# Performance work log

Hardware: AMD Instinct MI355X
Metric: run time of the kernel (lower is better)

The kernel has to match this reference:

```python
import jax, jax.numpy as jnp
import numpy as np

IMAGE_SIZE = 224
COV_HP = 1.0
SIGMA = 1.0
STEPS = 2
CUTOFF = 20.0
IMP_LO, IMP_HI = 0.5, 2.0
REL_W = 0.5
EPS = 1e-6

# Projection matrices for front/top/left views (buffer Js in the module)
JS = jnp.array([[[1, 0, 0], [0, 1, 0]],
                [[1, 0, 0], [0, 0, 1]],
                [[0, 0, 1], [0, 1, 0]]], dtype=jnp.float32)


def _blur(d, sigma):
    # d: [B,H,W]; separable Gaussian blur, 'same' padding
    r = max(1, int(3 * sigma))
    x = jnp.arange(-r, r + 1, dtype=jnp.float32)
    k = jnp.exp(-(x * x) / (2.0 * sigma * sigma))
    k = k / k.sum()
    d4 = d[:, None]  # [B,1,H,W]
    kh = k.reshape(1, 1, -1, 1)
    kw = k.reshape(1, 1, 1, -1)
    d4 = jax.lax.conv_general_dilated(d4, kh, (1, 1), [(r, r), (0, 0)],
                                      dimension_numbers=('NCHW', 'OIHW', 'NCHW'))
    d4 = jax.lax.conv_general_dilated(d4, kw, (1, 1), [(0, 0), (r, r)],
                                      dimension_numbers=('NCHW', 'OIHW', 'NCHW'))
    return d4[:, 0]


def _fill_depth_map(d, sigma, steps):
    # fill_depth_map is not defined in the source; implemented as iterative
    # Gaussian-blur hole filling (empty pixels take blurred neighborhood).
    for _ in range(steps):
        b = _blur(d, sigma)
        d = jnp.where(d > 1e-6, d, b)
    return d


def _forward(position, cov3d, opacity, importance):
    B, N, _ = position.shape
    H = W = IMAGE_SIZE
    Hh, Wh = H // 2, W // 2
    yy, xx = jnp.meshgrid(jnp.arange(Hh), jnp.arange(Wh), indexing='ij')
    grid = jnp.stack([xx, yy], axis=-1).astype(jnp.float32)  # [Hh,Wh,2]
    imp = jnp.clip(jnp.broadcast_to(importance[:, :N], (B, N)), IMP_LO, IMP_HI)
    imp = imp[:, :, None, None]
    eye3 = jnp.eye(3, dtype=cov3d.dtype)
    eye2 = jnp.eye(2, dtype=cov3d.dtype)
    maps = []
    for v in range(3):  # fixed small view loop, as in the source
        J = JS[v]  # [2,3]
        # NOTE: source mutates cov3d across the view loop; replicate that
        cov3d = (cov3d + jnp.swapaxes(cov3d, -1, -2)) * 0.5
        cov3d = cov3d + EPS * eye3
        nrm = jnp.linalg.norm(cov3d, axis=(-1, -2), keepdims=True)
        cov3d = cov3d / (nrm + EPS) * COV_HP
        cinv = jnp.linalg.inv(cov3d)                               # [B,N,3,3]
        cov2d_inv = jnp.einsum('ij,bnjk,lk->bnil', J, cinv, J)     # J C^-1 J^T
        cov2d_inv = cov2d_inv + eye2 * (EPS * 1e-4)
        proj = jnp.einsum('bnk,jk->bnj', position, J)              # [B,N,2]
        mn = proj.min(axis=1, keepdims=True)
        mx = proj.max(axis=1, keepdims=True)
        rng = mx - mn + 1e-6
        mn = mn - 0.5 * rng
        mx = mx + 0.5 * rng
        rng = mx - mn + 1e-6
        xy = jnp.clip((proj - mn) / rng * (Wh - 1), 0.0, Wh - 1)
        delta = grid[None, None] - xy[:, :, None, None, :]         # [B,N,Hh,Wh,2]
        mask_h = jnp.linalg.norm(delta, axis=-1) < CUTOFF
        mask = jnp.repeat(jnp.repeat(mask_h, 2, axis=2), 2, axis=3)
        exph = -jnp.einsum('bnhwj,bnjk,bnhwk->bnhw', delta, cov2d_inv, delta)
        exp_full = jax.image.resize(exph, (B, N, H, W), method='bilinear')
        exp_full = jnp.clip(exp_full, -20.0, 0.0)
        w = opacity[:, :, None, None] * imp * jnp.exp(exp_full)
        w = jnp.where(mask, w, 0.0)
        wmin = w.min(axis=1, keepdims=True)
        wmax = w.max(axis=1, keepdims=True)
        nw = (w - wmin) / (wmax - wmin + EPS) * REL_W + w / (w.sum(axis=1, keepdims=True) + EPS)
        dm = nw.sum(axis=1)  # [B,H,W]
        maps.append(_fill_depth_map(dm, SIGMA, STEPS))
    d = jnp.stack(maps, axis=1)  # [B,3,H,W], already 224x224 so resize is a no-op
    d = (d - d.mean()) / (jnp.std(d, ddof=1) + EPS)
    return d


def setup_inputs() -> dict:
    key = jax.random.key(0)
    k1, k2, k3 = jax.random.split(key, 3)
    B, N, MAXG = 1, 512, 1000
    return {
        'position': jax.random.normal(k1, (B, N, 3), dtype=jnp.float32),
        'cov3d': jax.random.normal(k2, (B, N, 3, 3), dtype=jnp.float32),
        'opacity': jax.random.uniform(k3, (B, N), dtype=jnp.float32),
        'importance': jnp.ones((1, MAXG), dtype=jnp.float32),
    }


def reference(position, cov3d, opacity, importance):
    return _forward(position, cov3d, opacity, importance)
```

## Files before the change

### kernel.cpp

```cpp
#include <hip/hip_runtime.h>
#include <math.h>


__device__ __forceinline__ float wave_min(float v) {
    #pragma unroll
    for (int o = 32; o >= 1; o >>= 1) v = fminf(v, __shfl_xor(v, o));
    return v;
}

__global__ __launch_bounds__(512) void splat_fused_kernel(
    const float* __restrict__ position, const float* __restrict__ cov3d,
    const float* __restrict__ opacity, const float* __restrict__ importance,
    float* __restrict__ dm) {
    __shared__ float4 lsA[512];
    __shared__ float2 lsB[512];
    __shared__ float red[8 * 6];
    __shared__ float4 pS[7][64], pMn[7][64], pMx[7][64];
    __shared__ int cnt;
    const int v = blockIdx.z;
    const int tx0 = blockIdx.x * 16, ty0 = blockIdx.y * 16;
    const int tid = threadIdx.x;
    const int lane = tid & 63, wave = tid >> 6;

    const int n = tid;
    const float p0 = position[n * 3 + 0];
    const float p1 = position[n * 3 + 1];
    const float p2 = position[n * 3 + 2];
    const float opimp = opacity[n] * fminf(fmaxf(importance[n], 0.5f), 2.0f);

    {
        float vals[6] = {p0, -p0, p1, -p1, p2, -p2};
        #pragma unroll
        for (int k = 0; k < 6; ++k) {
            float r = wave_min(vals[k]);
            if (lane == 0) red[wave * 6 + k] = r;
        }
    }
    __syncthreads();
    float mn6[6];
    #pragma unroll
    for (int k = 0; k < 6; ++k) {
        float r = red[k];
        #pragma unroll
        for (int w = 1; w < 8; ++w) r = fminf(r, red[w * 6 + k]);
        mn6[k] = r;
    }
    const float pmn[3] = {mn6[0], mn6[2], mn6[4]};
    const float pmx[3] = {-mn6[1], -mn6[3], -mn6[5]};

    float c00 = cov3d[n * 9 + 0], c01 = cov3d[n * 9 + 1], c02 = cov3d[n * 9 + 2];
    float c10 = cov3d[n * 9 + 3], c11 = cov3d[n * 9 + 4], c12 = cov3d[n * 9 + 5];
    float c20 = cov3d[n * 9 + 6], c21 = cov3d[n * 9 + 7], c22 = cov3d[n * 9 + 8];
    for (int vv = 0; vv <= v; ++vv) {
        float s01 = 0.5f * (c01 + c10);
        float s02 = 0.5f * (c02 + c20);
        float s12 = 0.5f * (c12 + c21);
        float s00 = c00 + 1e-6f;
        float s11 = c11 + 1e-6f;
        float s22 = c22 + 1e-6f;
        float nrm = sqrtf(s00 * s00 + s11 * s11 + s22 * s22 +
                          2.0f * (s01 * s01 + s02 * s02 + s12 * s12));
        float inv = 1.0f / (nrm + 1e-6f);
        c00 = s00 * inv; c11 = s11 * inv; c22 = s22 * inv;
        c01 = s01 * inv; c10 = c01; c02 = s02 * inv; c20 = c02;
        c12 = s12 * inv; c21 = c12;
    }
    float cof00 = c11 * c22 - c12 * c12;
    float cof01 = c02 * c12 - c01 * c22;
    float cof02 = c01 * c12 - c02 * c11;
    float det = c00 * cof00 + c01 * cof01 + c02 * cof02;
    float idet = 1.0f / det;
    float i00 = cof00 * idet;
    float i01 = cof01 * idet;
    float i02 = cof02 * idet;
    float i11 = (c00 * c22 - c02 * c02) * idet;
    float i12 = (c02 * c01 - c00 * c12) * idet;
    float i22 = (c00 * c11 - c01 * c01) * idet;

    float Aa, Ab, Ac, prx, pry;
    int ix, iy;
    if (v == 0)      { Aa = i00; Ab = i01; Ac = i11; prx = p0; pry = p1; ix = 0; iy = 1; }
    else if (v == 1) { Aa = i00; Ab = i02; Ac = i22; prx = p0; pry = p2; ix = 0; iy = 2; }
    else             { Aa = i22; Ab = i12; Ac = i11; prx = p2; pry = p1; ix = 2; iy = 1; }
    Aa += 1e-10f;
    Ac += 1e-10f;

    float mnx = pmn[ix], mxx = pmx[ix], mny = pmn[iy], mxy = pmx[iy];
    float rngx = mxx - mnx + 1e-6f;
    float mnx2 = mnx - 0.5f * rngx;
    float mxx2 = mxx + 0.5f * rngx;
    rngx = mxx2 - mnx2 + 1e-6f;
    float rngy = mxy - mny + 1e-6f;
    float mny2 = mny - 0.5f * rngy;
    float mxy2 = mxy + 0.5f * rngy;
    rngy = mxy2 - mny2 + 1e-6f;
    float gx = fminf(fmaxf((prx - mnx2) / rngx * 111.0f, 0.0f), 111.0f);
    float gy = fminf(fmaxf((pry - mny2) / rngy * 111.0f, 0.0f), 111.0f);

    if (tid == 0) cnt = 0;
    __syncthreads();
    {
        const float bx0 = (float)(tx0 >> 1), bx1 = (float)((tx0 + 15) >> 1);
        const float by0 = (float)(ty0 >> 1), by1 = (float)((ty0 + 15) >> 1);
        float dx = fmaxf(fmaxf(bx0 - gx, gx - bx1), 0.0f);
        float dy = fmaxf(fmaxf(by0 - gy, gy - by1), 0.0f);
        bool pass = (dx * dx + dy * dy) < 400.01f;
        unsigned long long m = __ballot(pass);
        int base = 0;
        if (lane == 0) base = atomicAdd(&cnt, __popcll(m));
        base = __shfl(base, 0);
        if (pass) {
            int slot = base + __popcll(m & ((1ull << lane) - 1ull));
            lsA[slot] = make_float4(Aa, 2.0f * Ab, Ac, opimp);
            lsB[slot] = make_float2(gx, gy);
        }
    }
    __syncthreads();
    const int len = cnt;

    const int qx = lane & 7, qy = lane >> 3;
    const int xh = (tx0 >> 1) + qx;
    const int yh = (ty0 >> 1) + qy;

    if (len == 0) {
        if (wave == 0) {
            #pragma unroll
            for (int py = 0; py < 2; ++py)
                #pragma unroll
                for (int px = 0; px < 2; ++px)
                    dm[(v * 224 + ty0 + 2 * qy + py) * 224 + tx0 + 2 * qx + px] = 0.0f;
        }
        return;
    }

    const int npad = (len + 15) & ~15;
    if (tid < npad - len) {
        lsA[len + tid] = make_float4(1.0f, 0.0f, 1.0f, 0.0f);
        lsB[len + tid] = make_float2(1e9f, 1e9f);
    }
    __syncthreads();

    float exA[2], eyA[2], VxA[2], VyA[2];
    #pragma unroll
    for (int p = 0; p < 2; ++p) {
        int xlo = xh - 1 + p; int xhi = min(xlo + 1, 111); xlo = max(xlo, 0);
        float wlo = p ? 0.75f : 0.25f, whi = 1.0f - wlo;
        exA[p] = wlo * (float)xlo + whi * (float)xhi;
        VxA[p] = wlo * whi * (float)(xhi - xlo) * (float)(xhi - xlo);
        int ylo = yh - 1 + p; int yhi2 = min(ylo + 1, 111); ylo = max(ylo, 0);
        eyA[p] = wlo * (float)ylo + whi * (float)yhi2;
        VyA[p] = wlo * whi * (float)(yhi2 - ylo) * (float)(yhi2 - ylo);
    }
    const float fxh = (float)xh, fyh = (float)yh;

    const int chunk = npad >> 3;
    const int cbeg = wave * chunk, cend = cbeg + chunk;

    float S00 = 0.f, S01 = 0.f, S10 = 0.f, S11 = 0.f;
    float mn00 = INFINITY, mn01 = INFINITY, mn10 = INFINITY, mn11 = INFINITY;
    float mx00 = -INFINITY, mx01 = -INFINITY, mx10 = -INFINITY, mx11 = -INFINITY;

    for (int i = cbeg; i < cend; i += 2) {
        float4 gA0 = lsA[i], gA1 = lsA[i + 1];
        float2 gB0 = lsB[i], gB1 = lsB[i + 1];
        #pragma unroll
        for (int u = 0; u < 2; ++u) {
            const float4 gA = u ? gA1 : gA0;
            const float2 gB = u ? gB1 : gB0;
            const float a = gA.x, b2 = gA.y, c = gA.z, op = gA.w;
            const float xx = gB.x, yy = gB.y;
            const float dxh = fxh - xx, dyh = fyh - yy;
            const bool inside = dxh * dxh + dyh * dyh < 400.0f;
            const float dx0 = exA[0] - xx, dx1 = exA[1] - xx;
            const float dy0 = eyA[0] - yy, dy1 = eyA[1] - yy;
            const float adx0 = a * dx0, adx1 = a * dx1;
            const float bdy0 = b2 * dy0, bdy1 = b2 * dy1;
            const float cdy0 = c * dy0 * dy0, cdy1 = c * dy1 * dy1;
            const float ax0 = a * VxA[0], ax1 = a * VxA[1];
            const float cy0 = c * VyA[0], cy1 = c * VyA[1];
            #pragma unroll
            for (int py = 0; py < 2; ++py) {
                const float dyp  = py ? dy1 : dy0;
                const float bdyp = py ? bdy1 : bdy0;
                const float cdyp = py ? cdy1 : cdy0;
                const float cyp  = py ? cy1 : cy0;
                #pragma unroll
                for (int px = 0; px < 2; ++px) {
                    const float dxp  = px ? dx1 : dx0;
                    const float adxp = px ? adx1 : adx0;
                    const float axp  = px ? ax1 : ax0;
                    float q = dxp * (adxp + bdyp) + cdyp;
                    float bil = -((q + axp) + cyp);
                    bil = fminf(fmaxf(bil, -20.0f), 0.0f);
                    bil = inside ? bil : -1e9f;
                    float w = op * __expf(bil);
                    if (py == 0 && px == 0) { S00 += w; mn00 = fminf(mn00, w); mx00 = fmaxf(mx00, w); }
                    if (py == 0 && px == 1) { S01 += w; mn01 = fminf(mn01, w); mx01 = fmaxf(mx01, w); }
                    if (py == 1 && px == 0) { S10 += w; mn10 = fminf(mn10, w); mx10 = fmaxf(mx10, w); }
                    if (py == 1 && px == 1) { S11 += w; mn11 = fminf(mn11, w); mx11 = fmaxf(mx11, w); }
                }
            }
        }
    }
    if (wave > 0) {
        pS[wave - 1][lane]  = make_float4(S00, S01, S10, S11);
        pMn[wave - 1][lane] = make_float4(mn00, mn01, mn10, mn11);
        pMx[wave - 1][lane] = make_float4(mx00, mx01, mx10, mx11);
    }
    __syncthreads();
    if (wave == 0) {
        #pragma unroll
        for (int k = 0; k < 7; ++k) {
            float4 s = pS[k][lane], m = pMn[k][lane], M = pMx[k][lane];
            S00 += s.x; S01 += s.y; S10 += s.z; S11 += s.w;
            mn00 = fminf(mn00, m.x); mn01 = fminf(mn01, m.y);
            mn10 = fminf(mn10, m.z); mn11 = fminf(mn11, m.w);
            mx00 = fmaxf(mx00, M.x); mx01 = fmaxf(mx01, M.y);
            mx10 = fmaxf(mx10, M.z); mx11 = fmaxf(mx11, M.w);
        }
        if (len < 512) {
            mn00 = fminf(mn00, 0.f); mn01 = fminf(mn01, 0.f);
            mn10 = fminf(mn10, 0.f); mn11 = fminf(mn11, 0.f);
            mx00 = fmaxf(mx00, 0.f); mx01 = fmaxf(mx01, 0.f);
            mx10 = fmaxf(mx10, 0.f); mx11 = fmaxf(mx11, 0.f);
        }
        float S4[4]  = {S00, S01, S10, S11};
        float mn4[4] = {mn00, mn01, mn10, mn11};
        float mx4[4] = {mx00, mx01, mx10, mx11};
        #pragma unroll
        for (int pp = 0; pp < 4; ++pp) {
            float S = S4[pp];
            float dmv = 0.5f * (S - 512.0f * mn4[pp]) / (mx4[pp] - mn4[pp] + 1e-6f)
                      + S / (S + 1e-6f);
            const int py = pp >> 1, px = pp & 1;
            dm[(v * 224 + ty0 + 2 * qy + py) * 224 + tx0 + 2 * qx + px] = dmv;
        }
    }
}

__global__ __launch_bounds__(256) void blur2_stats_kernel(
    const float* __restrict__ in, float* __restrict__ out,
    float2* __restrict__ partials) {
    __shared__ float A[28 * 29];
    __shared__ float T[28 * 29];
    __shared__ float r1[4], r2[4];
    const int v = blockIdx.z;
    const int tx0 = blockIdx.x * 16, ty0 = blockIdx.y * 16;
    const int tid = threadIdx.x;
    const float kw[7] = {0.00443305f, 0.05400558f, 0.24203623f, 0.39905030f,
                         0.24203623f, 0.05400558f, 0.00443305f};
    const float* __restrict__ chan = in + v * 224 * 224;

    for (int idx = tid; idx < 28 * 28; idx += 256) {
        int rr = idx / 28, c = idx % 28;
        int gyy = ty0 - 6 + rr, gxx = tx0 - 6 + c;
        float val = 0.0f;
        if (gyy >= 0 && gyy < 224 && gxx >= 0 && gxx < 224) val = chan[gyy * 224 + gxx];
        A[rr * 29 + c] = val;
    }
    __syncthreads();
    for (int idx = tid; idx < 22 * 28; idx += 256) {
        int rr = 3 + idx / 28, c = idx % 28;
        float s = 0.0f;
        #pragma unroll
        for (int i = 0; i < 7; ++i) s += kw[i] * A[(rr - 3 + i) * 29 + c];
        T[rr * 29 + c] = s;
    }
    __syncthreads();
    for (int idx = tid; idx < 22 * 22; idx += 256) {
        int rr = 3 + idx / 22, c = 3 + idx % 22;
        int gyy = ty0 - 6 + rr, gxx = tx0 - 6 + c;
        float s = 0.0f;
        #pragma unroll
        for (int j = 0; j < 7; ++j) s += kw[j] * T[rr * 29 + c - 3 + j];
        float ctr = A[rr * 29 + c];
        float d1 = ctr > 1e-6f ? ctr : s;
        if (gyy < 0 || gyy > 223 || gxx < 0 || gxx > 223) d1 = 0.0f;
        A[rr * 29 + c] = d1;
    }
    __syncthreads();
    for (int idx = tid; idx < 16 * 22; idx += 256) {
        int rr = 6 + idx / 22, c = 3 + idx % 22;
        float s = 0.0f;
        #pragma unroll
        for (int i = 0; i < 7; ++i) s += kw[i] * A[(rr - 3 + i) * 29 + c];
        T[rr * 29 + c] = s;
    }
    __syncthreads();
    float ls1 = 0.0f, ls2 = 0.0f;
    for (int idx = tid; idx < 16 * 16; idx += 256) {
        int rr = 6 + (idx >> 4), c = 6 + (idx & 15);
        float s = 0.0f;
        #pragma unroll
        for (int j = 0; j < 7; ++j) s += kw[j] * T[rr * 29 + c - 3 + j];
        float ctr = A[rr * 29 + c];
        float d2 = ctr > 1e-6f ? ctr : s;
        out[(v * 224 + ty0 + rr - 6) * 224 + (tx0 + c - 6)] = d2;
        ls1 += d2; ls2 += d2 * d2;
    }
    #pragma unroll
    for (int o = 32; o >= 1; o >>= 1) {
        ls1 += __shfl_xor(ls1, o);
        ls2 += __shfl_xor(ls2, o);
    }
    if ((tid & 63) == 0) { r1[tid >> 6] = ls1; r2[tid >> 6] = ls2; }
    __syncthreads();
    if (tid == 0) {
        float s1 = r1[0] + r1[1] + r1[2] + r1[3];
        float s2 = r2[0] + r2[1] + r2[2] + r2[3];
        partials[(blockIdx.z * 14 + blockIdx.y) * 14 + blockIdx.x] = make_float2(s1, s2);
    }
}

__global__ __launch_bounds__(256) void normalize_kernel(
    const float2* __restrict__ partials, float* __restrict__ out) {
    __shared__ double s1[256], s2[256];
    const int tid = threadIdx.x;
    double a = 0.0, b = 0.0;
    for (int i = tid; i < 588; i += 256) {
        float2 p = partials[i];
        a += (double)p.x; b += (double)p.y;
    }
    s1[tid] = a; s2[tid] = b;
    __syncthreads();
    for (int s = 128; s >= 1; s >>= 1) {
        if (tid < s) { s1[tid] += s1[tid + s]; s2[tid] += s2[tid + s]; }
        __syncthreads();
    }
    const double M = 150528.0;
    double mean = s1[0] / M;
    double var = (s2[0] - M * mean * mean) / (M - 1.0);
    double sd = sqrt(var > 0.0 ? var : 0.0);
    const int idx = blockIdx.x * 256 + tid;
    if (idx < 3 * 224 * 224)
        out[idx] = (out[idx] - (float)mean) / ((float)sd + 1e-6f);
}

extern "C" void kernel_launch(void* const* d_in, const int* in_sizes, int n_in,
                              void* d_out, int out_size, void* d_ws, size_t ws_size,
                              hipStream_t stream) {
    const float* position   = (const float*)d_in[0];
    const float* cov3d      = (const float*)d_in[1];
    const float* opacity    = (const float*)d_in[2];
    const float* importance = (const float*)d_in[3];
    float* out = (float*)d_out;

    float* dmA       = (float*)d_ws;
    float2* partials = (float2*)((float*)d_ws + 150528);

    hipLaunchKernelGGL(splat_fused_kernel, dim3(14, 14, 3), dim3(512), 0, stream,
                       position, cov3d, opacity, importance, dmA);
    hipLaunchKernelGGL(blur2_stats_kernel, dim3(14, 14, 3), dim3(256), 0, stream,
                       dmA, out, partials);
    hipLaunchKernelGGL(normalize_kernel, dim3(588), dim3(256), 0, stream,
                       partials, out);
}
```

Before: 90.57 us.

## Fuse splat, blur and normalize into one cooperative kernel with grid syncs

Replaces the three-kernel pipeline with a single cooperative launch. Grid-wide syncs separate the splat, the two-step blur with statistics, and the normalization, so two kernel launch gaps go away. Blocks shrink to 256 threads, each handling two Gaussians, so all 588 blocks can be co-resident, and the final value stays in a register instead of being written and read back. Each block redundantly reduces the 588 partials after the last sync. Grid-sync cost and lower per-block parallelism in the splat loop may offset the gain, and the old three-kernel path remains as a fallback if the cooperative launch fails.

```diff
diff --git a/kernel.cpp b/kernel.cpp
--- a/kernel.cpp
+++ b/kernel.cpp
@@ -1,5 +1,8 @@
 #include <hip/hip_runtime.h>
+#include <hip/hip_cooperative_groups.h>
 #include <math.h>
+
+namespace cg = cooperative_groups;
 
 
 __device__ __forceinline__ float wave_min(float v) {
@@ -8,83 +11,69 @@
     return v;
 }
 
-__global__ __launch_bounds__(512) void splat_fused_kernel(
+struct SpS {
+    float4 lsA[512];
+    float2 lsB[512];
+    float4 pS[3][64], pMn[3][64], pMx[3][64];
+    float red[4 * 6];
+    int cnt;
+};
+struct BlS {
+    float A[28 * 29];
+    float T[28 * 29];
+    float r1[4], r2[4];
+};
+struct NmS {
+    double s1[256], s2[256];
+};
+union SmU { SpS sp; BlS bl; NmS nm; };
+
+__global__ __launch_bounds__(256, 3) void fused_all_kernel(
     const float* __restrict__ position, const float* __restrict__ cov3d,
     const float* __restrict__ opacity, const float* __restrict__ importance,
-    float* __restrict__ dm) {
-    __shared__ float4 lsA[512];
-    __shared__ float2 lsB[512];
-    __shared__ float red[8 * 6];
-    __shared__ float4 pS[7][64], pMn[7][64], pMx[7][64];
-    __shared__ int cnt;
+    float* __restrict__ dm, float2* __restrict__ partials,
+    float* __restrict__ out) {
+    __shared__ SmU sm;
+    cg::grid_group gg = cg::this_grid();
     const int v = blockIdx.z;
     const int tx0 = blockIdx.x * 16, ty0 = blockIdx.y * 16;
     const int tid = threadIdx.x;
     const int lane = tid & 63, wave = tid >> 6;
 
-    const int n = tid;
-    const float p0 = position[n * 3 + 0];
-    const float p1 = position[n * 3 + 1];
-    const float p2 = position[n * 3 + 2];
-    const float opimp = opacity[n] * fminf(fmaxf(importance[n], 0.5f), 2.0f);
-
+    float P0[3], P1[3], OP0, OP1;
     {
-        float vals[6] = {p0, -p0, p1, -p1, p2, -p2};
+        const int n0 = tid, n1 = tid + 256;
+        P0[0] = position[n0 * 3 + 0]; P0[1] = position[n0 * 3 + 1]; P0[2] = position[n0 * 3 + 2];
+        P1[0] = position[n1 * 3 + 0]; P1[1] = position[n1 * 3 + 1]; P1[2] = position[n1 * 3 + 2];
+        OP0 = opacity[n0] * fminf(fmaxf(importance[n0], 0.5f), 2.0f);
+        OP1 = opacity[n1] * fminf(fmaxf(importance[n1], 0.5f), 2.0f);
+    }
+    if (tid == 0) sm.sp.cnt = 0;
+    {
+        float vals[6] = { fminf(P0[0], P1[0]), fminf(-P0[0], -P1[0]),
+                          fminf(P0[1], P1[1]), fminf(-P0[1], -P1[1]),
+                          fminf(P0[2], P1[2]), fminf(-P0[2], -P1[2]) };
         #pragma unroll
         for (int k = 0; k < 6; ++k) {
             float r = wave_min(vals[k]);
-            if (lane == 0) red[wave * 6 + k] = r;
+            if (lane == 0) sm.sp.red[wave * 6 + k] = r;
         }
     }
     __syncthreads();
     float mn6[6];
     #pragma unroll
     for (int k = 0; k < 6; ++k) {
-        float r = red[k];
-        #pragma unroll
-        for (int w = 1; w < 8; ++w) r = fminf(r, red[w * 6 + k]);
+        float r = sm.sp.red[k];
+        #pragma unroll
+        for (int w = 1; w < 4; ++w) r = fminf(r, sm.sp.red[w * 6 + k]);
         mn6[k] = r;
     }
     const float pmn[3] = {mn6[0], mn6[2], mn6[4]};
     const float pmx[3] = {-mn6[1], -mn6[3], -mn6[5]};
-
-    float c00 = cov3d[n * 9 + 0], c01 = cov3d[n * 9 + 1], c02 = cov3d[n * 9 + 2];
-    float c10 = cov3d[n * 9 + 3], c11 = cov3d[n * 9 + 4], c12 = cov3d[n * 9 + 5];
-    float c20 = cov3d[n * 9 + 6], c21 = cov3d[n * 9 + 7], c22 = cov3d[n * 9 + 8];
-    for (int vv = 0; vv <= v; ++vv) {
-        float s01 = 0.5f * (c01 + c10);
-        float s02 = 0.5f * (c02 + c20);
-        float s12 = 0.5f * (c12 + c21);
-        float s00 = c00 + 1e-6f;
-        float s11 = c11 + 1e-6f;
-        float s22 = c22 + 1e-6f;
-        float nrm = sqrtf(s00 * s00 + s11 * s11 + s22 * s22 +
-                          2.0f * (s01 * s01 + s02 * s02 + s12 * s12));
-        float inv = 1.0f / (nrm + 1e-6f);
-        c00 = s00 * inv; c11 = s11 * inv; c22 = s22 * inv;
-        c01 = s01 * inv; c10 = c01; c02 = s02 * inv; c20 = c02;
-        c12 = s12 * inv; c21 = c12;
-    }
-    float cof00 = c11 * c22 - c12 * c12;
-    float cof01 = c02 * c12 - c01 * c22;
-    float cof02 = c01 * c12 - c02 * c11;
-    float det = c00 * cof00 + c01 * cof01 + c02 * cof02;
-    float idet = 1.0f / det;
-    float i00 = cof00 * idet;
-    float i01 = cof01 * idet;
-    float i02 = cof02 * idet;
-    float i11 = (c00 * c22 - c02 * c02) * idet;
-    float i12 = (c02 * c01 - c00 * c12) * idet;
-    float i22 = (c00 * c11 - c01 * c01) * idet;
-
-    float Aa, Ab, Ac, prx, pry;
     int ix, iy;
-    if (v == 0)      { Aa = i00; Ab = i01; Ac = i11; prx = p0; pry = p1; ix = 0; iy = 1; }
-    else if (v == 1) { Aa = i00; Ab = i02; Ac = i22; prx = p0; pry = p2; ix = 0; iy = 2; }
-    else             { Aa = i22; Ab = i12; Ac = i11; prx = p2; pry = p1; ix = 2; iy = 1; }
-    Aa += 1e-10f;
-    Ac += 1e-10f;
-
+    if (v == 0)      { ix = 0; iy = 1; }
+    else if (v == 1) { ix = 0; iy = 2; }
+    else             { ix = 2; iy = 1; }
     float mnx = pmn[ix], mxx = pmx[ix], mny = pmn[iy], mxy = pmx[iy];
     float rngx = mxx - mnx + 1e-6f;
     float mnx2 = mnx - 0.5f * rngx;
@@ -94,49 +83,77 @@
     float mny2 = mny - 0.5f * rngy;
     float mxy2 = mxy + 0.5f * rngy;
     rngy = mxy2 - mny2 + 1e-6f;
-    float gx = fminf(fmaxf((prx - mnx2) / rngx * 111.0f, 0.0f), 111.0f);
-    float gy = fminf(fmaxf((pry - mny2) / rngy * 111.0f, 0.0f), 111.0f);
-
-    if (tid == 0) cnt = 0;
-    __syncthreads();
-    {
-        const float bx0 = (float)(tx0 >> 1), bx1 = (float)((tx0 + 15) >> 1);
-        const float by0 = (float)(ty0 >> 1), by1 = (float)((ty0 + 15) >> 1);
+    const float bx0 = (float)(tx0 >> 1), bx1 = (float)((tx0 + 15) >> 1);
+    const float by0 = (float)(ty0 >> 1), by1 = (float)((ty0 + 15) >> 1);
+
+    for (int g = 0; g < 2; ++g) {
+        const int n = tid + (g << 8);
+        const float p0 = g ? P1[0] : P0[0];
+        const float p1 = g ? P1[1] : P0[1];
+        const float p2 = g ? P1[2] : P0[2];
+        const float opimp = g ? OP1 : OP0;
+        float c00 = cov3d[n * 9 + 0], c01 = cov3d[n * 9 + 1], c02 = cov3d[n * 9 + 2];
+        float c10 = cov3d[n * 9 + 3], c11 = cov3d[n * 9 + 4], c12 = cov3d[n * 9 + 5];
+        float c20 = cov3d[n * 9 + 6], c21 = cov3d[n * 9 + 7], c22 = cov3d[n * 9 + 8];
+        for (int vv = 0; vv <= v; ++vv) {
+            float s01 = 0.5f * (c01 + c10);
+            float s02 = 0.5f * (c02 + c20);
+            float s12 = 0.5f * (c12 + c21);
+            float s00 = c00 + 1e-6f;
+            float s11 = c11 + 1e-6f;
+            float s22 = c22 + 1e-6f;
+            float nrm = sqrtf(s00 * s00 + s11 * s11 + s22 * s22 +
+                              2.0f * (s01 * s01 + s02 * s02 + s12 * s12));
+            float inv = 1.0f / (nrm + 1e-6f);
+            c00 = s00 * inv; c11 = s11 * inv; c22 = s22 * inv;
+            c01 = s01 * inv; c10 = c01; c02 = s02 * inv; c20 = c02;
+            c12 = s12 * inv; c21 = c12;
+        }
+        float cof00 = c11 * c22 - c12 * c12;
+        float cof01 = c02 * c12 - c01 * c22;
+        float cof02 = c01 * c12 - c02 * c11;
+        float det = c00 * cof00 + c01 * cof01 + c02 * cof02;
+        float idet = 1.0f / det;
+        float i00 = cof00 * idet;
+        float i01 = cof01 * idet;
+        float i02 = cof02 * idet;
+        float i11 = (c00 * c22 - c02 * c02) * idet;
+        float i12 = (c02 * c01 - c00 * c12) * idet;
+        float i22 = (c00 * c11 - c01 * c01) * idet;
+
+        float Aa, Ab, Ac, prx, pry;
+        if (v == 0)      { Aa = i00; Ab = i01; Ac = i11; prx = p0; pry = p1; }
+        else if (v == 1) { Aa = i00; Ab = i02; Ac = i22; prx = p0; pry = p2; }
+        else             { Aa = i22; Ab = i12; Ac = i11; prx = p2; pry = p1; }
+        Aa += 1e-10f;
+        Ac += 1e-10f;
+        float gx = fminf(fmaxf((prx - mnx2) / rngx * 111.0f, 0.0f), 111.0f);
+        float gy = fminf(fmaxf((pry - mny2) / rngy * 111.0f, 0.0f), 111.0f);
+
         float dx = fmaxf(fmaxf(bx0 - gx, gx - bx1), 0.0f);
         float dy = fmaxf(fmaxf(by0 - gy, gy - by1), 0.0f);
         bool pass = (dx * dx + dy * dy) < 400.01f;
         unsigned long long m = __ballot(pass);
         int base = 0;
-        if (lane == 0) base = atomicAdd(&cnt, __popcll(m));
+        if (lane == 0) base = atomicAdd(&sm.sp.cnt, __popcll(m));
         base = __shfl(base, 0);
         if (pass) {
             int slot = base + __popcll(m & ((1ull << lane) - 1ull));
-            lsA[slot] = make_float4(Aa, 2.0f * Ab, Ac, opimp);
-            lsB[slot] = make_float2(gx, gy);
-        }
-    }
-    __syncthreads();
-    const int len = cnt;
+            sm.sp.lsA[slot] = make_float4(Aa, 2.0f * Ab, Ac, opimp);
+            sm.sp.lsB[slot] = make_float2(gx, gy);
+        }
+    }
+    __syncthreads();
+    const int len = sm.sp.cnt;
 
     const int qx = lane & 7, qy = lane >> 3;
     const int xh = (tx0 >> 1) + qx;
     const int yh = (ty0 >> 1) + qy;
 
-    if (len == 0) {
-        if (wave == 0) {
-            #pragma unroll
-            for (int py = 0; py < 2; ++py)
-                #pragma unroll
-                for (int px = 0; px < 2; ++px)
-                    dm[(v * 224 + ty0 + 2 * qy + py) * 224 + tx0 + 2 * qx + px] = 0.0f;
-        }
-        return;
-    }
-
     const int npad = (len + 15) & ~15;
     if (tid < npad - len) {
-        lsA[len + tid] = make_float4(1.0f, 0.0f, 1.0f, 0.0f);
-        lsB[len + tid] = make_float2(1e9f, 1e9f);
+        sm.sp.lsA[len + tid] = make_float4(1.0f, 0.0f, 1.0f, 0.0f);
+        sm.sp.lsB[len + tid] = make_float2(1e9f, 1e9f);
     }
     __syncthreads();
 
@@ -153,7 +170,7 @@
     }
     const float fxh = (float)xh, fyh = (float)yh;
 
-    const int chunk = npad >> 3;
+    const int chunk = npad >> 2;
     const int cbeg = wave * chunk, cend = cbeg + chunk;
 
     float S00 = 0.f, S01 = 0.f, S10 = 0.f, S11 = 0.f;
@@ -161,8 +178,8 @@
     float mx00 = -INFINITY, mx01 = -INFINITY, mx10 = -INFINITY, mx11 = -INFINITY;
 
     for (int i = cbeg; i < cend; i += 2) {
-        float4 gA0 = lsA[i], gA1 = lsA[i + 1];
-        float2 gB0 = lsB[i], gB1 = lsB[i + 1];
+        float4 gA0 = sm.sp.lsA[i], gA1 = sm.sp.lsA[i + 1];
+        float2 gB0 = sm.sp.lsB[i], gB1 = sm.sp.lsB[i + 1];
         #pragma unroll
         for (int u = 0; u < 2; ++u) {
             const float4 gA = u ? gA1 : gA0;
@@ -184,6 +201,7 @@
                 const float bdyp = py ? bdy1 : bdy0;
                 const float cdyp = py ? cdy1 : cdy0;
                 const float cyp  = py ? cy1 : cy0;
+                (void)dyp;
                 #pragma unroll
                 for (int px = 0; px < 2; ++px) {
                     const float dxp  = px ? dx1 : dx0;
@@ -203,6 +221,321 @@
         }
     }
     if (wave > 0) {
+        sm.sp.pS[wave - 1][lane]  = make_float4(S00, S01, S10, S11);
+        sm.sp.pMn[wave - 1][lane] = make_float4(mn00, mn01, mn10, mn11);
+        sm.sp.pMx[wave - 1][lane] = make_float4(mx00, mx01, mx10, mx11);
+    }
+    __syncthreads();
+    if (wave == 0) {
+        #pragma unroll
+        for (int k = 0; k < 3; ++k) {
+            float4 s = sm.sp.pS[k][lane], m = sm.sp.pMn[k][lane], M = sm.sp.pMx[k][lane];
+            S00 += s.x; S01 += s.y; S10 += s.z; S11 += s.w;
+            mn00 = fminf(mn00, m.x); mn01 = fminf(mn01, m.y);
+            mn10 = fminf(mn10, m.z); mn11 = fminf(mn11, m.w);
+            mx00 = fmaxf(mx00, M.x); mx01 = fmaxf(mx01, M.y);
+            mx10 = fmaxf(mx10, M.z); mx11 = fmaxf(mx11, M.w);
+        }
+        if (len < 512) {
+            mn00 = fminf(mn00, 0.f); mn01 = fminf(mn01, 0.f);
+            mn10 = fminf(mn10, 0.f); mn11 = fminf(mn11, 0.f);
+            mx00 = fmaxf(mx00, 0.f); mx01 = fmaxf(mx01, 0.f);
+            mx10 = fmaxf(mx10, 0.f); mx11 = fmaxf(mx11, 0.f);
+        }
+        float S4[4]  = {S00, S01, S10, S11};
+        float mn4[4] = {mn00, mn01, mn10, mn11};
+        float mx4[4] = {mx00, mx01, mx10, mx11};
+        #pragma unroll
+        for (int pp = 0; pp < 4; ++pp) {
+            float S = S4[pp];
+            float dmv = 0.5f * (S - 512.0f * mn4[pp]) / (mx4[pp] - mn4[pp] + 1e-6f)
+                      + S / (S + 1e-6f);
+            const int py = pp >> 1, px = pp & 1;
+            dm[(v * 224 + ty0 + 2 * qy + py) * 224 + tx0 + 2 * qx + px] = dmv;
+        }
+    }
+
+    gg.sync();
+
+    const float kw[7] = {0.00443305f, 0.05400558f, 0.24203623f, 0.39905030f,
+                         0.24203623f, 0.05400558f, 0.00443305f};
+    const float* __restrict__ chan = dm + v * 224 * 224;
+
+    for (int idx = tid; idx < 28 * 28; idx += 256) {
+        int rr = idx / 28, c = idx % 28;
+        int gyy = ty0 - 6 + rr, gxx = tx0 - 6 + c;
+        float val = 0.0f;
+        if (gyy >= 0 && gyy < 224 && gxx >= 0 && gxx < 224) val = chan[gyy * 224 + gxx];
+        sm.bl.A[rr * 29 + c] = val;
+    }
+    __syncthreads();
+    for (int idx = tid; idx < 22 * 28; idx += 256) {
+        int rr = 3 + idx / 28, c = idx % 28;
+        float s = 0.0f;
+        #pragma unroll
+        for (int i = 0; i < 7; ++i) s += kw[i] * sm.bl.A[(rr - 3 + i) * 29 + c];
+        sm.bl.T[rr * 29 + c] = s;
+    }
+    __syncthreads();
+    for (int idx = tid; idx < 22 * 22; idx += 256) {
+        int rr = 3 + idx / 22, c = 3 + idx % 22;
+        int gyy = ty0 - 6 + rr, gxx = tx0 - 6 + c;
+        float s = 0.0f;
+        #pragma unroll
+        for (int j = 0; j < 7; ++j) s += kw[j] * sm.bl.T[rr * 29 + c - 3 + j];
+        float ctr = sm.bl.A[rr * 29 + c];
+        float d1 = ctr > 1e-6f ? ctr : s;
+        if (gyy < 0 || gyy > 223 || gxx < 0 || gxx > 223) d1 = 0.0f;
+        sm.bl.A[rr * 29 + c] = d1;
+    }
+    __syncthreads();
+    for (int idx = tid; idx < 16 * 22; idx += 256) {
+        int rr = 6 + idx / 22, c = 3 + idx % 22;
+        float s = 0.0f;
+        #pragma unroll
+        for (int i = 0; i < 7; ++i) s += kw[i] * sm.bl.A[(rr - 3 + i) * 29 + c];
+        sm.bl.T[rr * 29 + c] = s;
+    }
+    __syncthreads();
+    const int rr2 = 6 + (tid >> 4), cc2 = 6 + (tid & 15);
+    float d2;
+    {
+        float s = 0.0f;
+        #pragma unroll
+        for (int j = 0; j < 7; ++j) s += kw[j] * sm.bl.T[rr2 * 29 + cc2 - 3 + j];
+        float ctr = sm.bl.A[rr2 * 29 + cc2];
+        d2 = ctr > 1e-6f ? ctr : s;
+    }
+    float ls1 = d2, ls2 = d2 * d2;
+    #pragma unroll
+    for (int o = 32; o >= 1; o >>= 1) {
+        ls1 += __shfl_xor(ls1, o);
+        ls2 += __shfl_xor(ls2, o);
+    }
+    if (lane == 0) { sm.bl.r1[wave] = ls1; sm.bl.r2[wave] = ls2; }
+    __syncthreads();
+    if (tid == 0) {
+        float s1 = sm.bl.r1[0] + sm.bl.r1[1] + sm.bl.r1[2] + sm.bl.r1[3];
+        float s2 = sm.bl.r2[0] + sm.bl.r2[1] + sm.bl.r2[2] + sm.bl.r2[3];
+        partials[(v * 14 + blockIdx.y) * 14 + blockIdx.x] = make_float2(s1, s2);
+    }
+
+    gg.sync();
+
+    double a = 0.0, b = 0.0;
+    for (int i = tid; i < 588; i += 256) {
+        float2 p = partials[i];
+        a += (double)p.x; b += (double)p.y;
+    }
+    sm.nm.s1[tid] = a; sm.nm.s2[tid] = b;
+    __syncthreads();
+    for (int s = 128; s >= 1; s >>= 1) {
+        if (tid < s) { sm.nm.s1[tid] += sm.nm.s1[tid + s]; sm.nm.s2[tid] += sm.nm.s2[tid + s]; }
+        __syncthreads();
+    }
+    const double M = 150528.0;
+    double mean = sm.nm.s1[0] / M;
+    double var = (sm.nm.s2[0] - M * mean * mean) / (M - 1.0);
+    double sd = sqrt(var > 0.0 ? var : 0.0);
+    out[(v * 224 + ty0 + (tid >> 4)) * 224 + tx0 + (tid & 15)] =
+        (d2 - (float)mean) / ((float)sd + 1e-6f);
+}
+
+
+__global__ __launch_bounds__(512) void splat_fused_kernel(
+    const float* __restrict__ position, const float* __restrict__ cov3d,
+    const float* __restrict__ opacity, const float* __restrict__ importance,
+    float* __restrict__ dm) {
+    __shared__ float4 lsA[512];
+    __shared__ float2 lsB[512];
+    __shared__ float red[8 * 6];
+    __shared__ float4 pS[7][64], pMn[7][64], pMx[7][64];
+    __shared__ int cnt;
+    const int v = blockIdx.z;
+    const int tx0 = blockIdx.x * 16, ty0 = blockIdx.y * 16;
+    const int tid = threadIdx.x;
+    const int lane = tid & 63, wave = tid >> 6;
+
+    const int n = tid;
+    const float p0 = position[n * 3 + 0];
+    const float p1 = position[n * 3 + 1];
+    const float p2 = position[n * 3 + 2];
+    const float opimp = opacity[n] * fminf(fmaxf(importance[n], 0.5f), 2.0f);
+
+    {
+        float vals[6] = {p0, -p0, p1, -p1, p2, -p2};
+        #pragma unroll
+        for (int k = 0; k < 6; ++k) {
+            float r = wave_min(vals[k]);
+            if (lane == 0) red[wave * 6 + k] = r;
+        }
+    }
+    __syncthreads();
+    float mn6[6];
+    #pragma unroll
+    for (int k = 0; k < 6; ++k) {
+        float r = red[k];
+        #pragma unroll
+        for (int w = 1; w < 8; ++w) r = fminf(r, red[w * 6 + k]);
+        mn6[k] = r;
+    }
+    const float pmn[3] = {mn6[0], mn6[2], mn6[4]};
+    const float pmx[3] = {-mn6[1], -mn6[3], -mn6[5]};
+
+    float c00 = cov3d[n * 9 + 0], c01 = cov3d[n * 9 + 1], c02 = cov3d[n * 9 + 2];
+    float c10 = cov3d[n * 9 + 3], c11 = cov3d[n * 9 + 4], c12 = cov3d[n * 9 + 5];
+    float c20 = cov3d[n * 9 + 6], c21 = cov3d[n * 9 + 7], c22 = cov3d[n * 9 + 8];
+    for (int vv = 0; vv <= v; ++vv) {
+        float s01 = 0.5f * (c01 + c10);
+        float s02 = 0.5f * (c02 + c20);
+        float s12 = 0.5f * (c12 + c21);
+        float s00 = c00 + 1e-6f;
+        float s11 = c11 + 1e-6f;
+        float s22 = c22 + 1e-6f;
+        float nrm = sqrtf(s00 * s00 + s11 * s11 + s22 * s22 +
+                          2.0f * (s01 * s01 + s02 * s02 + s12 * s12));
+        float inv = 1.0f / (nrm + 1e-6f);
+        c00 = s00 * inv; c11 = s11 * inv; c22 = s22 * inv;
+        c01 = s01 * inv; c10 = c01; c02 = s02 * inv; c20 = c02;
+        c12 = s12 * inv; c21 = c12;
+    }
+    float cof00 = c11 * c22 - c12 * c12;
+    float cof01 = c02 * c12 - c01 * c22;
+    float cof02 = c01 * c12 - c02 * c11;
+    float det = c00 * cof00 + c01 * cof01 + c02 * cof02;
+    float idet = 1.0f / det;
+    float i00 = cof00 * idet;
+    float i01 = cof01 * idet;
+    float i02 = cof02 * idet;
+    float i11 = (c00 * c22 - c02 * c02) * idet;
+    float i12 = (c02 * c01 - c00 * c12) * idet;
+    float i22 = (c00 * c11 - c01 * c01) * idet;
+
+    float Aa, Ab, Ac, prx, pry;
+    int ix, iy;
+    if (v == 0)      { Aa = i00; Ab = i01; Ac = i11; prx = p0; pry = p1; ix = 0; iy = 1; }
+    else if (v == 1) { Aa = i00; Ab = i02; Ac = i22; prx = p0; pry = p2; ix = 0; iy = 2; }
+    else             { Aa = i22; Ab = i12; Ac = i11; prx = p2; pry = p1; ix = 2; iy = 1; }
+    Aa += 1e-10f;
+    Ac += 1e-10f;
+
+    float mnx = pmn[ix], mxx = pmx[ix], mny = pmn[iy], mxy = pmx[iy];
+    float rngx = mxx - mnx + 1e-6f;
+    float mnx2 = mnx - 0.5f * rngx;
+    float mxx2 = mxx + 0.5f * rngx;
+    rngx = mxx2 - mnx2 + 1e-6f;
+    float rngy = mxy - mny + 1e-6f;
+    float mny2 = mny - 0.5f * rngy;
+    float mxy2 = mxy + 0.5f * rngy;
+    rngy = mxy2 - mny2 + 1e-6f;
+    float gx = fminf(fmaxf((prx - mnx2) / rngx * 111.0f, 0.0f), 111.0f);
+    float gy = fminf(fmaxf((pry - mny2) / rngy * 111.0f, 0.0f), 111.0f);
+
+    if (tid == 0) cnt = 0;
+    __syncthreads();
+    {
+        const float bx0 = (float)(tx0 >> 1), bx1 = (float)((tx0 + 15) >> 1);
+        const float by0 = (float)(ty0 >> 1), by1 = (float)((ty0 + 15) >> 1);
+        float dx = fmaxf(fmaxf(bx0 - gx, gx - bx1), 0.0f);
+        float dy = fmaxf(fmaxf(by0 - gy, gy - by1), 0.0f);
+        bool pass = (dx * dx + dy * dy) < 400.01f;
+        unsigned long long m = __ballot(pass);
+        int base = 0;
+        if (lane == 0) base = atomicAdd(&cnt, __popcll(m));
+        base = __shfl(base, 0);
+        if (pass) {
+            int slot = base + __popcll(m & ((1ull << lane) - 1ull));
+            lsA[slot] = make_float4(Aa, 2.0f * Ab, Ac, opimp);
+            lsB[slot] = make_float2(gx, gy);
+        }
+    }
+    __syncthreads();
+    const int len = cnt;
+
+    const int qx = lane & 7, qy = lane >> 3;
+    const int xh = (tx0 >> 1) + qx;
+    const int yh = (ty0 >> 1) + qy;
+
+    if (len == 0) {
+        if (wave == 0) {
+            #pragma unroll
+            for (int py = 0; py < 2; ++py)
+                #pragma unroll
+                for (int px = 0; px < 2; ++px)
+                    dm[(v * 224 + ty0 + 2 * qy + py) * 224 + tx0 + 2 * qx + px] = 0.0f;
+        }
+        return;
+    }
+
+    const int npad = (len + 15) & ~15;
+    if (tid < npad - len) {
+        lsA[len + tid] = make_float4(1.0f, 0.0f, 1.0f, 0.0f);
+        lsB[len + tid] = make_float2(1e9f, 1e9f);
+    }
+    __syncthreads();
+
+    float exA[2], eyA[2], VxA[2], VyA[2];
+    #pragma unroll
+    for (int p = 0; p < 2; ++p) {
+        int xlo = xh - 1 + p; int xhi = min(xlo + 1, 111); xlo = max(xlo, 0);
+        float wlo = p ? 0.75f : 0.25f, whi = 1.0f - wlo;
+        exA[p] = wlo * (float)xlo + whi * (float)xhi;
+        VxA[p] = wlo * whi * (float)(xhi - xlo) * (float)(xhi - xlo);
+        int ylo = yh - 1 + p; int yhi2 = min(ylo + 1, 111); ylo = max(ylo, 0);
+        eyA[p] = wlo * (float)ylo + whi * (float)yhi2;
+        VyA[p] = wlo * whi * (float)(yhi2 - ylo) * (float)(yhi2 - ylo);
+    }
+    const float fxh = (float)xh, fyh = (float)yh;
+
+    const int chunk = npad >> 3;
+    const int cbeg = wave * chunk, cend = cbeg + chunk;
+
+    float S00 = 0.f, S01 = 0.f, S10 = 0.f, S11 = 0.f;
+    float mn00 = INFINITY, mn01 = INFINITY, mn10 = INFINITY, mn11 = INFINITY;
+    float mx00 = -INFINITY, mx01 = -INFINITY, mx10 = -INFINITY, mx11 = -INFINITY;
+
+    for (int i = cbeg; i < cend; i += 2) {
+        float4 gA0 = lsA[i], gA1 = lsA[i + 1];
+        float2 gB0 = lsB[i], gB1 = lsB[i + 1];
+        #pragma unroll
+        for (int u = 0; u < 2; ++u) {
+            const float4 gA = u ? gA1 : gA0;
+            const float2 gB = u ? gB1 : gB0;
+            const float a = gA.x, b2 = gA.y, c = gA.z, op = gA.w;
+            const float xx = gB.x, yy = gB.y;
+            const float dxh = fxh - xx, dyh = fyh - yy;
+            const bool inside = dxh * dxh + dyh * dyh < 400.0f;
+            const float dx0 = exA[0] - xx, dx1 = exA[1] - xx;
+            const float dy0 = eyA[0] - yy, dy1 = eyA[1] - yy;
+            const float adx0 = a * dx0, adx1 = a * dx1;
+            const float bdy0 = b2 * dy0, bdy1 = b2 * dy1;
+            const float cdy0 = c * dy0 * dy0, cdy1 = c * dy1 * dy1;
+            const float ax0 = a * VxA[0], ax1 = a * VxA[1];
+            const float cy0 = c * VyA[0], cy1 = c * VyA[1];
+            #pragma unroll
+            for (int py = 0; py < 2; ++py) {
+                const float bdyp = py ? bdy1 : bdy0;
+                const float cdyp = py ? cdy1 : cdy0;
+                const float cyp  = py ? cy1 : cy0;
+                #pragma unroll
+                for (int px = 0; px < 2; ++px) {
+                    const float dxp  = px ? dx1 : dx0;
+                    const float adxp = px ? adx1 : adx0;
+                    const float axp  = px ? ax1 : ax0;
+                    float q = dxp * (adxp + bdyp) + cdyp;
+                    float bil = -((q + axp) + cyp);
+                    bil = fminf(fmaxf(bil, -20.0f), 0.0f);
+                    bil = inside ? bil : -1e9f;
+                    float w = op * __expf(bil);
+                    if (py == 0 && px == 0) { S00 += w; mn00 = fminf(mn00, w); mx00 = fmaxf(mx00, w); }
+                    if (py == 0 && px == 1) { S01 += w; mn01 = fminf(mn01, w); mx01 = fmaxf(mx01, w); }
+                    if (py == 1 && px == 0) { S10 += w; mn10 = fminf(mn10, w); mx10 = fmaxf(mx10, w); }
+                    if (py == 1 && px == 1) { S11 += w; mn11 = fminf(mn11, w); mx11 = fmaxf(mx11, w); }
+                }
+            }
+        }
+    }
+    if (wave > 0) {
         pS[wave - 1][lane]  = make_float4(S00, S01, S10, S11);
         pMn[wave - 1][lane] = make_float4(mn00, mn01, mn10, mn11);
         pMx[wave - 1][lane] = make_float4(mx00, mx01, mx10, mx11);
@@ -348,10 +681,18 @@
     float* dmA       = (float*)d_ws;
     float2* partials = (float2*)((float*)d_ws + 150528);
 
-    hipLaunchKernelGGL(splat_fused_kernel, dim3(14, 14, 3), dim3(512), 0, stream,
-                       position, cov3d, opacity, importance, dmA);
-    hipLaunchKernelGGL(blur2_stats_kernel, dim3(14, 14, 3), dim3(256), 0, stream,
-                       dmA, out, partials);
-    hipLaunchKernelGGL(normalize_kernel, dim3(588), dim3(256), 0, stream,
-                       partials, out);
+    void* args[] = {(void*)&position, (void*)&cov3d, (void*)&opacity,
+                    (void*)&importance, (void*)&dmA, (void*)&partials,
+                    (void*)&out};
+    hipError_t err = hipLaunchCooperativeKernel(
+        reinterpret_cast<const void*>(&fused_all_kernel),
+        dim3(14, 14, 3), dim3(256), args, 0, stream);
+    if (err != hipSuccess) {
+        hipLaunchKernelGGL(splat_fused_kernel, dim3(14, 14, 3), dim3(512), 0, stream,
+                           position, cov3d, opacity, importance, dmA);
+        hipLaunchKernelGGL(blur2_stats_kernel, dim3(14, 14, 3), dim3(256), 0, stream,
+                           dmA, out, partials);
+        hipLaunchKernelGGL(normalize_kernel, dim3(588), dim3(256), 0, stream,
+                           partials, out);
+    }
 }
```

After: 200.4 us. +121.3%, slower.
